# Kernel tuning notes

Hardware: AMD Instinct MI355X
Metric: run time of the kernel (lower is better)

Reference implementation:

```python
import jax, jax.numpy as jnp
import numpy as np

INPUT_SIZE = 128
HIDDEN = 256
BATCH = 64
SEQ = 2048


def setup_inputs() -> dict:
    key = jax.random.key(0)
    k1, k2, k3, k4, k5 = jax.random.split(key, 5)
    bound = 1.0 / np.sqrt(HIDDEN)
    x = jax.random.normal(k1, (BATCH, SEQ, INPUT_SIZE), dtype=jnp.float32)
    W_ih = jax.random.uniform(k2, (4 * HIDDEN, INPUT_SIZE), minval=-bound, maxval=bound, dtype=jnp.float32)
    W_hh = jax.random.uniform(k3, (4 * HIDDEN, HIDDEN), minval=-bound, maxval=bound, dtype=jnp.float32)
    b_ih = jax.random.uniform(k4, (4 * HIDDEN,), minval=-bound, maxval=bound, dtype=jnp.float32)
    b_hh = jax.random.uniform(k5, (4 * HIDDEN,), minval=-bound, maxval=bound, dtype=jnp.float32)
    return {"x": x, "W_ih": W_ih, "W_hh": W_hh, "b_ih": b_ih, "b_hh": b_hh}


def reference(x, W_ih, W_hh, b_ih, b_hh):
    # Faithful to the source: lstm_cell is called WITHOUT previous state at every
    # step, so h_prev = c_prev = 0 for each timestep. W_hh @ h_prev == 0, and
    # f_gate * c_prev == 0. Each timestep is independent -> vectorize over time.
    H = W_hh.shape[1]
    # gates: [B, T, 4H]
    gates = jnp.einsum('bti,gi->btg', x, W_ih) + b_ih + b_hh
    i_g, f_g, g_g, o_g = jnp.split(gates, 4, axis=-1)  # PyTorch order: i, f, g, o
    i_g = jax.nn.sigmoid(i_g)
    g_g = jnp.tanh(g_g)
    o_g = jax.nn.sigmoid(o_g)
    c = i_g * g_g                      # f_g * c_prev == 0 since c_prev = 0
    h = o_g * jnp.tanh(c)
    return (h, c)
```

## Files before the change

### kernel.cpp

```cpp
#include <hip/hip_runtime.h>
#include <hip/hip_bf16.h>


#define M_TOTAL (64 * 2048)
#define K_DIM   128
#define N_OUT   256
#define NBLOCKS 1024

typedef __bf16 bf16x8 __attribute__((ext_vector_type(8)));
typedef float  f32x16 __attribute__((ext_vector_type(16)));

static __device__ __forceinline__ bf16x8 cvt8(float4 a, float4 b) {
    bf16x8 r;
    r[0] = (__bf16)a.x; r[1] = (__bf16)a.y; r[2] = (__bf16)a.z; r[3] = (__bf16)a.w;
    r[4] = (__bf16)b.x; r[5] = (__bf16)b.y; r[6] = (__bf16)b.z; r[7] = (__bf16)b.w;
    return r;
}

static __device__ __forceinline__ float fast_sigmoid(float x) {
    float e = __expf(-x);
    return __builtin_amdgcn_rcpf(1.0f + e);
}

static __device__ __forceinline__ float fast_tanh(float x) {
    float e = __expf(2.0f * x);
    return 1.0f - 2.0f * __builtin_amdgcn_rcpf(e + 1.0f);
}

__global__ __launch_bounds__(256, 2)
void lstm_gates_kernel(const float* __restrict__ x,
                       const float* __restrict__ Wih,
                       const float* __restrict__ bih,
                       const float* __restrict__ bhh,
                       float* __restrict__ hout,
                       float* __restrict__ cout)
{
    const int lane  = threadIdx.x & 63;
    const int wid   = threadIdx.x >> 6;
    const int gw    = blockIdx.x * 4 + wid;
    const int cs    = gw & 7;
    const int grp   = gw >> 3;
    const int ngrp  = (NBLOCKS * 4) >> 3;

    const int c0    = cs * 32;
    const int ln31  = lane & 31;
    const int khalf = (lane >> 5) * 8;

    bf16x8 bi[8], bg[8], bo[8];
    {
        const float4* wi = (const float4*)(Wih + (size_t)(0   + c0 + ln31) * K_DIM + khalf);
        const float4* wg = (const float4*)(Wih + (size_t)(512 + c0 + ln31) * K_DIM + khalf);
        const float4* wo = (const float4*)(Wih + (size_t)(768 + c0 + ln31) * K_DIM + khalf);
        #pragma unroll
        for (int kk = 0; kk < 8; ++kk) {
            bi[kk] = cvt8(wi[kk * 4], wi[kk * 4 + 1]);
            bg[kk] = cvt8(wg[kk * 4], wg[kk * 4 + 1]);
            bo[kk] = cvt8(wo[kk * 4], wo[kk * 4 + 1]);
        }
    }
    const float bias_i = bih[0   + c0 + ln31] + bhh[0   + c0 + ln31];
    const float bias_g = bih[512 + c0 + ln31] + bhh[512 + c0 + ln31];
    const float bias_o = bih[768 + c0 + ln31] + bhh[768 + c0 + ln31];

    for (int t = grp; t < M_TOTAL / 32; t += ngrp) {
        const int m0 = t * 32;
        const float4* ap = (const float4*)(x + (size_t)(m0 + ln31) * K_DIM + khalf);
        bf16x8 a[8];
        #pragma unroll
        for (int kk = 0; kk < 8; ++kk)
            a[kk] = cvt8(ap[kk * 4], ap[kk * 4 + 1]);

        f32x16 ai = (f32x16)0.0f, ag = (f32x16)0.0f, ao = (f32x16)0.0f;
        #pragma unroll
        for (int kk = 0; kk < 8; ++kk) {
            ai = __builtin_amdgcn_mfma_f32_32x32x16_bf16(a[kk], bi[kk], ai, 0, 0, 0);
            ag = __builtin_amdgcn_mfma_f32_32x32x16_bf16(a[kk], bg[kk], ag, 0, 0, 0);
            ao = __builtin_amdgcn_mfma_f32_32x32x16_bf16(a[kk], bo[kk], ao, 0, 0, 0);
        }

        #pragma unroll
        for (int r = 0; r < 16; ++r) {
            const int row = m0 + (r & 3) + 8 * (r >> 2) + 4 * (lane >> 5);
            float vi = ai[r] + bias_i;
            float vg = ag[r] + bias_g;
            float vo = ao[r] + bias_o;
            float si = fast_sigmoid(vi);
            float tg = fast_tanh(vg);
            float so = fast_sigmoid(vo);
            float c  = si * tg;
            float tc = fast_tanh(c);
            float h  = so * tc;
            const size_t off = (size_t)row * N_OUT + c0 + ln31;
            hout[off] = h;
            cout[off] = c;
        }
    }
}

extern "C" void kernel_launch(void* const* d_in, const int* in_sizes, int n_in,
                              void* d_out, int out_size, void* d_ws, size_t ws_size,
                              hipStream_t stream) {
    const float* x   = (const float*)d_in[0];
    const float* Wih = (const float*)d_in[1];
    const float* bih = (const float*)d_in[3];
    const float* bhh = (const float*)d_in[4];
    float* hout = (float*)d_out;
    float* cout = hout + (size_t)M_TOTAL * N_OUT;

    lstm_gates_kernel<<<NBLOCKS, 256, 0, stream>>>(x, Wih, bih, bhh, hout, cout);
}
```

Baseline: 399.1 us.

## Share x tiles via async global-to-LDS loads across 8 column-slice waves

Each 512-thread block now has 8 waves covering all 256 output columns. The waves share one 64-row x tile, which is loaded directly into swizzled LDS with global_load_lds and staged through a triple buffer so the next tile loads while the current one is computed. Before, each wave reloaded its x rows from global memory for its own 32-column slice, so x was read 8 times. The new version removes that redundant traffic at the cost of LDS use, one barrier per iteration, and a fixed grid of 256 blocks.

```diff
diff --git a/kernel.cpp b/kernel.cpp
--- a/kernel.cpp
+++ b/kernel.cpp
@@ -1,11 +1,15 @@
 #include <hip/hip_runtime.h>
 #include <hip/hip_bf16.h>
+#include <stdint.h>
 
 
-#define M_TOTAL (64 * 2048)
-#define K_DIM   128
-#define N_OUT   256
-#define NBLOCKS 1024
+#define M_TOTAL   (64 * 2048)
+#define K_DIM     128
+#define N_OUT     256
+#define TILE_ROWS 64
+#define TILE_BYTES (TILE_ROWS * K_DIM * 4)
+#define NBLK      256
+#define ITERS     (M_TOTAL / TILE_ROWS / NBLK)
 
 typedef __bf16 bf16x8 __attribute__((ext_vector_type(8)));
 typedef float  f32x16 __attribute__((ext_vector_type(16)));
@@ -27,7 +31,13 @@
     return 1.0f - 2.0f * __builtin_amdgcn_rcpf(e + 1.0f);
 }
 
-__global__ __launch_bounds__(256, 2)
+static __device__ __forceinline__ void gload_lds16(const void* g, void* l) {
+    __builtin_amdgcn_global_load_lds(
+        (const __attribute__((address_space(1))) void*)g,
+        (__attribute__((address_space(3))) void*)l, 16, 0, 0);
+}
+
+__global__ __launch_bounds__(512, 2)
 void lstm_gates_kernel(const float* __restrict__ x,
                        const float* __restrict__ Wih,
                        const float* __restrict__ bih,
@@ -35,16 +45,15 @@
                        float* __restrict__ hout,
                        float* __restrict__ cout)
 {
-    const int lane  = threadIdx.x & 63;
-    const int wid   = threadIdx.x >> 6;
-    const int gw    = blockIdx.x * 4 + wid;
-    const int cs    = gw & 7;
-    const int grp   = gw >> 3;
-    const int ngrp  = (NBLOCKS * 4) >> 3;
+    __shared__ uint8_t lds[3 * TILE_BYTES];
 
-    const int c0    = cs * 32;
+    const int tid   = threadIdx.x;
+    const int lane  = tid & 63;
+    const int w     = tid >> 6;
+    const int c0    = w * 32;
     const int ln31  = lane & 31;
     const int khalf = (lane >> 5) * 8;
+    const uint32_t xr = (uint32_t)(ln31 & 7) << 4;
 
     bf16x8 bi[8], bg[8], bo[8];
     {
@@ -62,38 +71,64 @@
     const float bias_g = bih[512 + c0 + ln31] + bhh[512 + c0 + ln31];
     const float bias_o = bih[768 + c0 + ln31] + bhh[768 + c0 + ln31];
 
-    for (int t = grp; t < M_TOTAL / 32; t += ngrp) {
-        const int m0 = t * 32;
-        const float4* ap = (const float4*)(x + (size_t)(m0 + ln31) * K_DIM + khalf);
-        bf16x8 a[8];
+    const int t0 = blockIdx.x * ITERS;
+
+    auto stage = [&](int buf, int t) {
+        const uint8_t* gbase = (const uint8_t*)x + (size_t)t * TILE_BYTES;
+        uint8_t* lbase = lds + (size_t)buf * TILE_BYTES + (size_t)w * 4096;
         #pragma unroll
-        for (int kk = 0; kk < 8; ++kk)
-            a[kk] = cvt8(ap[kk * 4], ap[kk * 4 + 1]);
+        for (int j = 0; j < 4; ++j) {
+            uint32_t d   = (uint32_t)w * 4096u + (uint32_t)j * 1024u + (uint32_t)lane * 16u;
+            uint32_t src = d ^ (((d >> 9) & 7u) << 4);
+            gload_lds16(gbase + src, lbase + (uint32_t)j * 1024u);
+        }
+    };
 
-        f32x16 ai = (f32x16)0.0f, ag = (f32x16)0.0f, ao = (f32x16)0.0f;
+    auto compute = [&](int buf, int t) {
+        const uint8_t* lbase = lds + (size_t)buf * TILE_BYTES;
         #pragma unroll
-        for (int kk = 0; kk < 8; ++kk) {
-            ai = __builtin_amdgcn_mfma_f32_32x32x16_bf16(a[kk], bi[kk], ai, 0, 0, 0);
-            ag = __builtin_amdgcn_mfma_f32_32x32x16_bf16(a[kk], bg[kk], ag, 0, 0, 0);
-            ao = __builtin_amdgcn_mfma_f32_32x32x16_bf16(a[kk], bo[kk], ao, 0, 0, 0);
+        for (int s = 0; s < 2; ++s) {
+            const uint8_t* rowp = lbase + (uint32_t)(s * 32 + ln31) * 512u;
+            bf16x8 a[8];
+            #pragma unroll
+            for (int kk = 0; kk < 8; ++kk) {
+                const uint32_t off0 = (uint32_t)khalf * 4u + (uint32_t)kk * 64u;
+                float4 lo = *(const float4*)(rowp + ((off0      ) ^ xr));
+                float4 hi = *(const float4*)(rowp + ((off0 + 16u) ^ xr));
+                a[kk] = cvt8(lo, hi);
+            }
+            f32x16 ai = (f32x16)0.0f, ag = (f32x16)0.0f, ao = (f32x16)0.0f;
+            #pragma unroll
+            for (int kk = 0; kk < 8; ++kk) {
+                ai = __builtin_amdgcn_mfma_f32_32x32x16_bf16(a[kk], bi[kk], ai, 0, 0, 0);
+                ag = __builtin_amdgcn_mfma_f32_32x32x16_bf16(a[kk], bg[kk], ag, 0, 0, 0);
+                ao = __builtin_amdgcn_mfma_f32_32x32x16_bf16(a[kk], bo[kk], ao, 0, 0, 0);
+            }
+            const int m0 = t * TILE_ROWS + s * 32;
+            #pragma unroll
+            for (int r = 0; r < 16; ++r) {
+                const int row = m0 + (r & 3) + 8 * (r >> 2) + 4 * (lane >> 5);
+                float vi = ai[r] + bias_i;
+                float vg = ag[r] + bias_g;
+                float vo = ao[r] + bias_o;
+                float si = fast_sigmoid(vi);
+                float tg = fast_tanh(vg);
+                float so = fast_sigmoid(vo);
+                float c  = si * tg;
+                float tc = fast_tanh(c);
+                float h  = so * tc;
+                const size_t off = (size_t)row * N_OUT + c0 + ln31;
+                hout[off] = h;
+                cout[off] = c;
+            }
         }
+    };
 
-        #pragma unroll
-        for (int r = 0; r < 16; ++r) {
-            const int row = m0 + (r & 3) + 8 * (r >> 2) + 4 * (lane >> 5);
-            float vi = ai[r] + bias_i;
-            float vg = ag[r] + bias_g;
-            float vo = ao[r] + bias_o;
-            float si = fast_sigmoid(vi);
-            float tg = fast_tanh(vg);
-            float so = fast_sigmoid(vo);
-            float c  = si * tg;
-            float tc = fast_tanh(c);
-            float h  = so * tc;
-            const size_t off = (size_t)row * N_OUT + c0 + ln31;
-            hout[off] = h;
-            cout[off] = c;
-        }
+    stage(0, t0);
+    for (int i = 0; i < ITERS; ++i) {
+        __syncthreads();
+        if (i + 1 < ITERS) stage((i + 1) % 3, t0 + i + 1);
+        compute(i % 3, t0 + i);
     }
 }
 
@@ -107,5 +142,5 @@
     float* hout = (float*)d_out;
     float* cout = hout + (size_t)M_TOTAL * N_OUT;
 
-    lstm_gates_kernel<<<NBLOCKS, 256, 0, stream>>>(x, Wih, bih, bhh, hout, cout);
+    lstm_gates_kernel<<<NBLK, 512, 0, stream>>>(x, Wih, bih, bhh, hout, cout);
 }
```

Measured after the change: 339.8 us. 14.9% less time.
